# Performance work log

Measured on AMD Instinct MI355X. Metric: run time of the kernel, lower is better.

The kernel has to match this reference:

```python
import jax, jax.numpy as jnp
import numpy as np

B, T, D = 4096, 200, 64
H = 32  # hidden units of score MLP
NEG_INF = jnp.float32(-2**32 + 1)


def setup_inputs() -> dict:
    key = jax.random.key(0)
    k1, k2, k3, k4, k5 = jax.random.split(key, 5)
    query = jax.random.normal(k1, (B, 1, D), dtype=jnp.float32)
    keys = jax.random.normal(k2, (B, T, D), dtype=jnp.float32)
    mask = jax.random.randint(k3, (B, T), 0, 2) > 0
    mask = mask.at[:, 0].set(True)  # ensure at least one valid key per row
    # Glorot-normal-ish init for the tiny score MLP
    W1 = jax.random.normal(k4, (3 * D, H), dtype=jnp.float32) * jnp.sqrt(2.0 / (3 * D + H))
    b1 = jnp.zeros((H,), dtype=jnp.float32)
    W2 = jax.random.normal(k5, (H, 1), dtype=jnp.float32) * jnp.sqrt(2.0 / (H + 1))
    b2 = jnp.zeros((1,), dtype=jnp.float32)
    return {"query": query, "keys": keys, "mask": mask,
            "W1": W1, "b1": b1, "W2": W2, "b2": b2}


def reference(query, keys, mask, W1, b1, W2, b2):
    b, t, d = keys.shape
    q = jnp.broadcast_to(query, (b, t, d))            # tile query over seq
    att_in = jnp.concatenate([q, keys, q - keys], axis=-1)   # [B,T,3D]
    h = jax.nn.sigmoid(att_in @ W1 + b1)              # [B,T,H]
    score = (h @ W2 + b2)[..., 0]                     # [B,T]
    score = jnp.where(mask, score, NEG_INF)
    w = jax.nn.softmax(score, axis=-1)                # [B,T]
    out = jnp.einsum('bt,btd->bd', w, keys)           # weighted key sum
    return out[:, None, :]                            # [B,1,D]
```

## Files before the change

kernel.cpp:

```cpp
#include <hip/hip_runtime.h>
#include <hip/hip_bf16.h>


#define B 4096
#define T 200
#define D 64
#define H 32
#define LOG2E 1.44269504088896340736f
#define SOFF 16.0f
#define NTILE 13

typedef __attribute__((ext_vector_type(8))) short short8;
typedef __attribute__((ext_vector_type(4))) float f32x4;


__global__ __launch_bounds__(256) void prep_kernel(
        const float* __restrict__ W1,
        float*       __restrict__ ws)
{
    int n = blockIdx.x * 256 + threadIdx.x;
    if (blockIdx.x < 8) {
        int k = n >> 5;
        int j = n & 31;
        ws[n] = W1[k * H + j] + W1[(128 + k) * H + j];
    } else {
        int m = n - 2048;
        int e  = m & 7;
        int l  = (m >> 3) & 63;
        int fs = m >> 9;
        int ntile = fs >> 1, kstep = fs & 1;
        int k = kstep * 32 + (l >> 4) * 8 + e;
        int j = ntile * 16 + (l & 15);
        float v = W1[(64 + k) * H + j] - W1[(128 + k) * H + j];
        __hip_bfloat16 hv = __float2bfloat16(v);
        reinterpret_cast<unsigned short*>(ws + 2048)[m] =
            __builtin_bit_cast(unsigned short, hv);
    }
}

__device__ __forceinline__ unsigned short bf16u(float x) {
    __hip_bfloat16 h = __float2bfloat16(x);
    return __builtin_bit_cast(unsigned short, h);
}

__global__ __launch_bounds__(256) void attn_pool_kernel(
        const float* __restrict__ keys,
        const int*   __restrict__ mask,
        const unsigned short* __restrict__ wkf,
        const float* __restrict__ wsum,
        const float* __restrict__ b1,
        const float* __restrict__ W2,
        const float* __restrict__ query,
        float*       __restrict__ out)
{
    __shared__ float qsh[4][64];
    __shared__ float part[4][68];

    const int tid  = threadIdx.x;
    const int wv   = tid >> 6;
    const int lane = tid & 63;
    const int quad = lane >> 4;
    const int l15  = lane & 15;

    const int b = (blockIdx.x & 7) * (B / 8) + (blockIdx.x >> 3);

    qsh[wv][lane] = query[(size_t)b * D + lane];
    const int jq = lane & 31;
    const int kh = lane >> 5;
    float qac0 = kh ? 0.0f : b1[jq];
    float qac1 = 0.0f;
    #pragma unroll
    for (int k0 = 0; k0 < 32; k0 += 2) {
        int k = kh * 32 + k0;
        qac0 = fmaf(qsh[wv][k],     wsum[k * H + jq],       qac0);
        qac1 = fmaf(qsh[wv][k + 1], wsum[(k + 1) * H + jq], qac1);
    }
    float qac = qac0 + qac1;
    qac += __shfl_xor(qac, 32, 64);
    const float qa0 = __shfl(qac, l15, 64);
    const float qa1 = __shfl(qac, 16 + l15, 64);

    const short8* wf = reinterpret_cast<const short8*>(wkf);
    short8 bf0 = wf[0 * 64 + lane];
    short8 bf1 = wf[1 * 64 + lane];
    short8 bf2 = wf[2 * 64 + lane];
    short8 bf3 = wf[3 * 64 + lane];
    const float w20 = W2[l15];
    const float w21 = W2[16 + l15];

    const float4* krow = reinterpret_cast<const float4*>(keys + (size_t)b * (T * D));
    const int*    mrow = mask + (size_t)b * T;
    const int ib = quad * 2;

    float acc[16];
    #pragma unroll
    for (int j = 0; j < 16; ++j) acc[j] = 0.0f;
    float dacc = 0.0f;

    const int ntl = (wv == 0) ? 4 : 3;

    float4 kA0 = krow[(wv * 16 + l15) * 16 + ib + 0];
    float4 kA1 = krow[(wv * 16 + l15) * 16 + ib + 1];
    float4 kA2 = krow[(wv * 16 + l15) * 16 + 8 + ib + 0];
    float4 kA3 = krow[(wv * 16 + l15) * 16 + 8 + ib + 1];
    int    mA  = mrow[wv * 16 + l15];

    #pragma unroll 1
    for (int it = 0; it < ntl; ++it) {
        const int tile = wv + it * 4;
        float4 kB0 = kA0, kB1 = kA1, kB2 = kA2, kB3 = kA3;
        int    mB  = mA;
        if (it + 1 < ntl) {
            int tn  = (wv + (it + 1) * 4) * 16 + l15;
            int trn = (tn < T) ? tn : (T - 1);
            kB0 = krow[trn * 16 + ib + 0];
            kB1 = krow[trn * 16 + ib + 1];
            kB2 = krow[trn * 16 + 8 + ib + 0];
            kB3 = krow[trn * 16 + 8 + ib + 1];
            mB  = mrow[trn];
        }

        short8 a0, a1;
        a0[0] = (short)bf16u(kA0.x); a0[1] = (short)bf16u(kA0.y);
        a0[2] = (short)bf16u(kA0.z); a0[3] = (short)bf16u(kA0.w);
        a0[4] = (short)bf16u(kA1.x); a0[5] = (short)bf16u(kA1.y);
        a0[6] = (short)bf16u(kA1.z); a0[7] = (short)bf16u(kA1.w);
        a1[0] = (short)bf16u(kA2.x); a1[1] = (short)bf16u(kA2.y);
        a1[2] = (short)bf16u(kA2.z); a1[3] = (short)bf16u(kA2.w);
        a1[4] = (short)bf16u(kA3.x); a1[5] = (short)bf16u(kA3.y);
        a1[6] = (short)bf16u(kA3.z); a1[7] = (short)bf16u(kA3.w);

        f32x4 c0 = {0.f, 0.f, 0.f, 0.f};
        f32x4 c1 = {0.f, 0.f, 0.f, 0.f};
        c0 = __builtin_amdgcn_mfma_f32_16x16x32_bf16(a0, bf0, c0, 0, 0, 0);
        c0 = __builtin_amdgcn_mfma_f32_16x16x32_bf16(a1, bf1, c0, 0, 0, 0);
        c1 = __builtin_amdgcn_mfma_f32_16x16x32_bf16(a0, bf2, c1, 0, 0, 0);
        c1 = __builtin_amdgcn_mfma_f32_16x16x32_bf16(a1, bf3, c1, 0, 0, 0);

        float p[4];
        #pragma unroll
        for (int r = 0; r < 4; ++r) {
            float x0 = c0[r] + qa0;
            float x1 = c1[r] + qa1;
            float s0 = __builtin_amdgcn_rcpf(1.0f + exp2f(-x0 * LOG2E));
            float s1 = __builtin_amdgcn_rcpf(1.0f + exp2f(-x1 * LOG2E));
            p[r] = fmaf(s0, w20, s1 * w21);
        }
        #pragma unroll
        for (int r = 0; r < 4; ++r) {
            #pragma unroll
            for (int off = 1; off <= 8; off <<= 1)
                p[r] += __shfl_xor(p[r], off, 64);
        }
        const int addr = (l15 >> 2) << 6;
        int q0 = __builtin_amdgcn_ds_bpermute(addr, __builtin_bit_cast(int, p[0]));
        int q1 = __builtin_amdgcn_ds_bpermute(addr, __builtin_bit_cast(int, p[1]));
        int q2 = __builtin_amdgcn_ds_bpermute(addr, __builtin_bit_cast(int, p[2]));
        int q3 = __builtin_amdgcn_ds_bpermute(addr, __builtin_bit_cast(int, p[3]));
        const int rsel = l15 & 3;
        int s01 = (rsel & 1) ? q1 : q0;
        int s23 = (rsel & 1) ? q3 : q2;
        float st = __builtin_bit_cast(float, (rsel & 2) ? s23 : s01);

        const int t = tile * 16 + l15;
        const float w = ((t < T) && (mA != 0)) ? exp2f((st - SOFF) * LOG2E) : 0.0f;

        acc[0]  = fmaf(w, kA0.x, acc[0]);  acc[1]  = fmaf(w, kA0.y, acc[1]);
        acc[2]  = fmaf(w, kA0.z, acc[2]);  acc[3]  = fmaf(w, kA0.w, acc[3]);
        acc[4]  = fmaf(w, kA1.x, acc[4]);  acc[5]  = fmaf(w, kA1.y, acc[5]);
        acc[6]  = fmaf(w, kA1.z, acc[6]);  acc[7]  = fmaf(w, kA1.w, acc[7]);
        acc[8]  = fmaf(w, kA2.x, acc[8]);  acc[9]  = fmaf(w, kA2.y, acc[9]);
        acc[10] = fmaf(w, kA2.z, acc[10]); acc[11] = fmaf(w, kA2.w, acc[11]);
        acc[12] = fmaf(w, kA3.x, acc[12]); acc[13] = fmaf(w, kA3.y, acc[13]);
        acc[14] = fmaf(w, kA3.z, acc[14]); acc[15] = fmaf(w, kA3.w, acc[15]);
        dacc += w;

        kA0 = kB0; kA1 = kB1; kA2 = kB2; kA3 = kB3; mA = mB;
    }

    #pragma unroll
    for (int j = 0; j < 16; ++j) {
        #pragma unroll
        for (int off = 1; off <= 8; off <<= 1)
            acc[j] += __shfl_xor(acc[j], off, 64);
    }
    #pragma unroll
    for (int off = 1; off <= 8; off <<= 1)
        dacc += __shfl_xor(dacc, off, 64);

    if (l15 == 0) {
        float4 o0 = {acc[0],  acc[1],  acc[2],  acc[3]};
        float4 o1 = {acc[4],  acc[5],  acc[6],  acc[7]};
        float4 o2 = {acc[8],  acc[9],  acc[10], acc[11]};
        float4 o3 = {acc[12], acc[13], acc[14], acc[15]};
        *reinterpret_cast<float4*>(&part[wv][quad * 8 + 0])      = o0;
        *reinterpret_cast<float4*>(&part[wv][quad * 8 + 4])      = o1;
        *reinterpret_cast<float4*>(&part[wv][32 + quad * 8 + 0]) = o2;
        *reinterpret_cast<float4*>(&part[wv][32 + quad * 8 + 4]) = o3;
    }
    if (lane == 0) part[wv][64] = dacc;
    __syncthreads();

    if (tid < 64) {
        float s  = (part[0][tid] + part[1][tid]) + (part[2][tid] + part[3][tid]);
        float dn = (part[0][64]  + part[1][64])  + (part[2][64]  + part[3][64]);
        out[(size_t)b * D + tid] = s * __builtin_amdgcn_rcpf(dn);
    }
}

extern "C" void kernel_launch(void* const* d_in, const int* in_sizes, int n_in,
                              void* d_out, int out_size, void* d_ws, size_t ws_size,
                              hipStream_t stream) {
    const float* query = (const float*)d_in[0];
    const float* keys  = (const float*)d_in[1];
    const int*   mask  = (const int*)d_in[2];
    const float* W1    = (const float*)d_in[3];
    const float* b1    = (const float*)d_in[4];
    const float* W2    = (const float*)d_in[5];

    float* ws = (float*)d_ws;
    float* wsum = ws;
    unsigned short* wkf = (unsigned short*)(ws + 2048);

    prep_kernel<<<16, 256, 0, stream>>>(W1, ws);
    attn_pool_kernel<<<B, 256, 0, stream>>>(keys, mask, wkf, wsum, b1, W2,
                                            query, (float*)d_out);
}
```

Before: 301.3 us.

## Stage key tiles via async global-to-LDS loads with swizzled double buffering

Key rows now go through a per-wave double-buffered LDS slab filled with global_load_lds 16-byte direct loads, using an XOR swizzle to avoid bank conflicts. The previous approach prefetched into registers. The next tile is issued before the current one is consumed, with an explicit vmcnt wait. The goal is fully coalesced row loads and less register pressure from the prefetch, at the cost of extra LDS traffic and 32KB of shared memory per block, which may limit occupancy. The block-to-batch remapping is also dropped in favour of the plain blockIdx order.

Measured after the change: 304.7 us. About the same (+1.1%).

```diff
diff --git a/kernel.cpp b/kernel.cpp
--- a/kernel.cpp
+++ b/kernel.cpp
@@ -43,6 +43,12 @@
     return __builtin_bit_cast(unsigned short, h);
 }
 
+__device__ __forceinline__ void gld16(const float* g, float* l) {
+    __builtin_amdgcn_global_load_lds(
+        (const __attribute__((address_space(1))) void*)g,
+        (__attribute__((address_space(3))) void*)l, 16, 0, 0);
+}
+
 __global__ __launch_bounds__(256) void attn_pool_kernel(
         const float* __restrict__ keys,
         const int*   __restrict__ mask,
@@ -53,6 +59,7 @@
         const float* __restrict__ query,
         float*       __restrict__ out)
 {
+    __shared__ float kslab[4][2][1024];
     __shared__ float qsh[4][64];
     __shared__ float part[4][68];
 
@@ -62,7 +69,7 @@
     const int quad = lane >> 4;
     const int l15  = lane & 15;
 
-    const int b = (blockIdx.x & 7) * (B / 8) + (blockIdx.x >> 3);
+    const int b = blockIdx.x;
 
     qsh[wv][lane] = query[(size_t)b * D + lane];
     const int jq = lane & 31;
@@ -88,9 +95,11 @@
     const float w20 = W2[l15];
     const float w21 = W2[16 + l15];
 
-    const float4* krow = reinterpret_cast<const float4*>(keys + (size_t)b * (T * D));
-    const int*    mrow = mask + (size_t)b * T;
-    const int ib = quad * 2;
+    const float* kbase = keys + (size_t)b * (T * D);
+    const int*   mrow  = mask + (size_t)b * T;
+
+    const int srow = lane >> 4;
+    const int sgi  = lane & 15;
 
     float acc[16];
     #pragma unroll
@@ -99,26 +108,47 @@
 
     const int ntl = (wv == 0) ? 4 : 3;
 
-    float4 kA0 = krow[(wv * 16 + l15) * 16 + ib + 0];
-    float4 kA1 = krow[(wv * 16 + l15) * 16 + ib + 1];
-    float4 kA2 = krow[(wv * 16 + l15) * 16 + 8 + ib + 0];
-    float4 kA3 = krow[(wv * 16 + l15) * 16 + 8 + ib + 1];
-    int    mA  = mrow[wv * 16 + l15];
-
+    int mA = mrow[wv * 16 + l15];
+    {
+        const int tb = wv * 16;
+        #pragma unroll
+        for (int i = 0; i < 4; ++i) {
+            int rl = i * 4 + srow;
+            int sg = (sgi & 8) | ((sgi ^ rl) & 7);
+            gld16(kbase + (size_t)(tb + rl) * D + sg * 4, &kslab[wv][0][i * 256]);
+        }
+    }
+
+    int cb = 0;
     #pragma unroll 1
     for (int it = 0; it < ntl; ++it) {
         const int tile = wv + it * 4;
-        float4 kB0 = kA0, kB1 = kA1, kB2 = kA2, kB3 = kA3;
-        int    mB  = mA;
-        if (it + 1 < ntl) {
-            int tn  = (wv + (it + 1) * 4) * 16 + l15;
-            int trn = (tn < T) ? tn : (T - 1);
-            kB0 = krow[trn * 16 + ib + 0];
-            kB1 = krow[trn * 16 + ib + 1];
-            kB2 = krow[trn * 16 + 8 + ib + 0];
-            kB3 = krow[trn * 16 + 8 + ib + 1];
-            mB  = mrow[trn];
-        }
+
+        int tn  = (tile + 4) * 16 + l15;
+        int trn = (tn < T) ? tn : (T - 1);
+        int mB  = mrow[trn];
+        {
+            const int tb = (tile + 4) * 16;
+            #pragma unroll
+            for (int i = 0; i < 4; ++i) {
+                int rl = i * 4 + srow;
+                int rg = tb + rl; if (rg >= T) rg = T - 1;
+                int sg = (sgi & 8) | ((sgi ^ rl) & 7);
+                gld16(kbase + (size_t)rg * D + sg * 4, &kslab[wv][cb ^ 1][i * 256]);
+            }
+        }
+
+        asm volatile("s_waitcnt vmcnt(4)" ::: "memory");
+        __builtin_amdgcn_sched_barrier(0);
+
+        const float* sl = kslab[wv][cb];
+        const int x   = l15 & 7;
+        const int gi0 = ((2 * quad)     ^ x) & 7;
+        const int gi1 = ((2 * quad + 1) ^ x) & 7;
+        float4 kA0 = *reinterpret_cast<const float4*>(&sl[l15 * 64 + gi0 * 4]);
+        float4 kA1 = *reinterpret_cast<const float4*>(&sl[l15 * 64 + gi1 * 4]);
+        float4 kA2 = *reinterpret_cast<const float4*>(&sl[l15 * 64 + 32 + gi0 * 4]);
+        float4 kA3 = *reinterpret_cast<const float4*>(&sl[l15 * 64 + 32 + gi1 * 4]);
 
         short8 a0, a1;
         a0[0] = (short)bf16u(kA0.x); a0[1] = (short)bf16u(kA0.y);
@@ -175,7 +205,8 @@
         acc[14] = fmaf(w, kA3.z, acc[14]); acc[15] = fmaf(w, kA3.w, acc[15]);
         dacc += w;
 
-        kA0 = kB0; kA1 = kB1; kA2 = kB2; kA3 = kB3; mA = mB;
+        mA = mB;
+        cb ^= 1;
     }
 
     #pragma unroll
```
